# Kernel optimization log

Hardware: AMD Instinct MI355X
Metric: run time of the kernel (lower is better)

The kernel has to match this reference:

```python
import jax, jax.numpy as jnp
import numpy as np

B, T, L, H = 512, 512, 64, 512  # batch, time_steps, sequence_len, hidden_dim


def gru_cell(x, h, W_ih, W_hh, b_ih, b_hh):
    # PyTorch GRUCell math. W_ih: [3H, in], W_hh: [3H, H]; gate order (r, z, n).
    gi = x @ W_ih.T + b_ih
    gh = h @ W_hh.T + b_hh
    i_r, i_z, i_n = jnp.split(gi, 3, axis=-1)
    h_r, h_z, h_n = jnp.split(gh, 3, axis=-1)
    r = jax.nn.sigmoid(i_r + h_r)
    z = jax.nn.sigmoid(i_z + h_z)
    n = jnp.tanh(i_n + r * h_n)
    return (1.0 - z) * n + z * h


def setup_inputs() -> dict:
    key = jax.random.key(0)
    ks = jax.random.split(key, 12)
    s = 1.0 / np.sqrt(H)  # PyTorch GRUCell/Linear init scale
    u = lambda k, shape: jax.random.uniform(k, shape, jnp.float32, -s, s)
    return {
        "x": jax.random.normal(ks[0], (B, T + L - 1), jnp.float32),
        "h_1": jnp.zeros((B, H), jnp.float32),
        "h_2": jnp.zeros((B, H), jnp.float32),
        "W_ih1": u(ks[1], (3 * H, T)),
        "W_hh1": u(ks[2], (3 * H, H)),
        "b_ih1": u(ks[3], (3 * H,)),
        "b_hh1": u(ks[4], (3 * H,)),
        "W_ih2": u(ks[5], (3 * H, H)),
        "W_hh2": u(ks[6], (3 * H, H)),
        "b_ih2": u(ks[7], (3 * H,)),
        "b_hh2": u(ks[8], (3 * H,)),
        "W_fc": u(ks[9], (1, H)),
        "b_fc": u(ks[10], (1,)),
    }


def reference(x, h_1, h_2, W_ih1, W_hh1, b_ih1, b_hh1,
              W_ih2, W_hh2, b_ih2, b_hh2, W_fc, b_fc):
    # Sliding windows x[:, t:t+T] for t in [0, L): gather once, scan over steps.
    idx = jnp.arange(L)[:, None] + jnp.arange(T)[None, :]  # [L, T]
    xs = jnp.transpose(x[:, idx], (1, 0, 2))  # [L, B, T]

    def step(carry, x_t):
        h1, h2 = carry
        h1 = gru_cell(x_t, h1, W_ih1, W_hh1, b_ih1, b_hh1)
        h2 = gru_cell(h1, h2, W_ih2, W_hh2, b_ih2, b_hh2)
        y = (h2 @ W_fc.T + b_fc)[:, 0]  # [B]
        return (h1, h2), y

    (h1, h2), ys = jax.lax.scan(step, (h_1, h_2), xs)
    return ys.T, h1, h2  # output_seq [B, L], final hidden states
```

## Files before the change

kernel.cpp:

```cpp
#include <hip/hip_runtime.h>
#include <hip/hip_bf16.h>
#include <math.h>

typedef __attribute__((ext_vector_type(8))) short short8;
typedef __attribute__((ext_vector_type(4))) float f32x4;
typedef unsigned short u16;
typedef unsigned int u32;

__device__ __forceinline__ u16 f2bf(float f) {
  union { float f; u32 u; } x; x.f = f;
  return (u16)((x.u + 0x7fffu + ((x.u >> 16) & 1u)) >> 16);
}
__device__ __forceinline__ float sigm(float v) { return 1.0f / (1.0f + __expf(-v)); }

#define MFMA __builtin_amdgcn_mfma_f32_16x16x32_bf16
#define HS 262144

#define LDG16_BODY(FL)                                        \
    "global_load_dwordx4 %0, %16, off " FL "\n\t"             \
    "global_load_dwordx4 %1, %16, off offset:64 " FL "\n\t"   \
    "global_load_dwordx4 %2, %16, off offset:128 " FL "\n\t"  \
    "global_load_dwordx4 %3, %16, off offset:192 " FL "\n\t"  \
    "global_load_dwordx4 %4, %16, off offset:256 " FL "\n\t"  \
    "global_load_dwordx4 %5, %16, off offset:320 " FL "\n\t"  \
    "global_load_dwordx4 %6, %16, off offset:384 " FL "\n\t"  \
    "global_load_dwordx4 %7, %16, off offset:448 " FL "\n\t"  \
    "global_load_dwordx4 %8, %16, off offset:512 " FL "\n\t"  \
    "global_load_dwordx4 %9, %16, off offset:576 " FL "\n\t"  \
    "global_load_dwordx4 %10, %16, off offset:640 " FL "\n\t" \
    "global_load_dwordx4 %11, %16, off offset:704 " FL "\n\t" \
    "global_load_dwordx4 %12, %16, off offset:768 " FL "\n\t" \
    "global_load_dwordx4 %13, %16, off offset:832 " FL "\n\t" \
    "global_load_dwordx4 %14, %16, off offset:896 " FL "\n\t" \
    "global_load_dwordx4 %15, %16, off offset:960 " FL "\n\t" \
    "s_waitcnt vmcnt(0)"
#define LDG16_OPS(a, base)                                                     \
    : "=&v"(a[0]), "=&v"(a[1]), "=&v"(a[2]), "=&v"(a[3]), "=&v"(a[4]),         \
      "=&v"(a[5]), "=&v"(a[6]), "=&v"(a[7]), "=&v"(a[8]), "=&v"(a[9]),         \
      "=&v"(a[10]), "=&v"(a[11]), "=&v"(a[12]), "=&v"(a[13]), "=&v"(a[14]),    \
      "=&v"(a[15])                                                             \
    : "v"(base) : "memory"

__device__ __forceinline__ void ldg16_sc0(short8 a[16], const u16* base) {
  asm volatile(LDG16_BODY("sc0") LDG16_OPS(a, base));
}
__device__ __forceinline__ void ldg16_sc01(short8 a[16], const u16* base) {
  asm volatile(LDG16_BODY("sc0 sc1") LDG16_OPS(a, base));
}
__device__ __forceinline__ void stg_sc01(u32* p, u32 v) {
  asm volatile("global_store_dword %0, %1, off sc0 sc1" :: "v"(p), "v"(v) : "memory");
}

__device__ __forceinline__ void waits_nf(unsigned* a, unsigned ta, unsigned* b, unsigned tb) {
  if (threadIdx.x == 0) {
    while (__hip_atomic_load(a, __ATOMIC_RELAXED, __HIP_MEMORY_SCOPE_AGENT) < ta)
      __builtin_amdgcn_s_sleep(1);
    while (__hip_atomic_load(b, __ATOMIC_RELAXED, __HIP_MEMORY_SCOPE_AGENT) < tb)
      __builtin_amdgcn_s_sleep(1);
  }
  __syncthreads();
}

__global__ __launch_bounds__(256, 1) void gru_fused(
    const float* __restrict__ xin, const float* __restrict__ h1in, const float* __restrict__ h2in,
    const float* __restrict__ Wih1, const float* __restrict__ Whh1,
    const float* __restrict__ bih1, const float* __restrict__ bhh1,
    const float* __restrict__ Wih2, const float* __restrict__ Whh2,
    const float* __restrict__ bih2, const float* __restrict__ bhh2,
    const float* __restrict__ Wfc, const float* __restrict__ bfc,
    float* __restrict__ out, u16* __restrict__ wsb, unsigned* __restrict__ barc)
{
  const int bid   = blockIdx.x;
  const int rb    = bid & 3;
  const int layer = (bid >> 2) & 1;
  const int cbl   = bid >> 3;
  const int n0    = cbl * 16;
  const int wid   = bid >> 2;
  const int tid   = threadIdx.x;
  const int w     = tid >> 6;
  const int lane  = tid & 63;
  const int quad  = lane >> 4;
  const int m16   = lane & 15;

  u16* x0  = wsb;
  u16* x1  = x0 + 512 * 576;
  u16* h1r = x1 + 512 * 576;
  u16* h2r = h1r + 4 * HS;
  u16* h1m = h2r + 4 * HS;

  __shared__ short8 wlds[96 * 64];

  unsigned* c0    = barc + rb * 32;
  unsigned* c1    = barc + 256 + rb * 32;
  unsigned* cinit = barc + 512;

  const float* Wih = layer ? Wih2 : Wih1;
  const float* Whh = layer ? Whh2 : Whh1;
  const float* bih = layer ? bih2 : bih1;
  const float* bhh = layer ? bhh2 : bhh1;

  for (int i = wid * 256 + tid; i < 128 * 575; i += 64 * 256) {
    int r = i / 575, c = i - r * 575;
    int row = rb * 128 + r;
    u16 bv = f2bf(xin[row * 575 + c]);
    x0[row * 576 + c] = bv;
    if (c >= 1) x1[row * 576 + (c - 1)] = bv;
  }
  for (int i = wid * 256 + tid; i < 128 * 512; i += 64 * 256) {
    int r = i >> 9, c = i & 511;
    int row = rb * 128 + r;
    u16 h1v = f2bf(h1in[row * 512 + c]);
    h1r[3 * HS + row * 512 + c] = h1v;
    h2r[3 * HS + row * 512 + c] = f2bf(h2in[row * 512 + c]);
  }
  for (int i = tid; i < 96 * 64; i += 256) {
    int blk = i >> 6, l = i & 63;
    int s, gr;
    if (blk < 64) { s = blk & 31; gr = (blk >> 5) * 512; }
    else          { s = blk - 64; gr = 1024; }
    int n  = n0 + (l & 15);
    int k0 = s * 32 + (l >> 4) * 8;
    short8 pk;
    #pragma unroll
    for (int j = 0; j < 8; ++j) {
      int k = k0 + j;
      float v = (k < 512) ? Wih[(gr + n) * 512 + k] : Whh[(gr + n) * 512 + (k - 512)];
      pk[j] = (short)f2bf(v);
    }
    wlds[blk * 64 + l] = pk;
  }

  float hreg[2][4];
  const float* hin = layer ? h2in : h1in;
  #pragma unroll
  for (int rf = 0; rf < 2; ++rf)
    #pragma unroll
    for (int q = 0; q < 4; ++q)
      hreg[rf][q] = hin[(rb * 128 + (2 * w + rf) * 16 + quad * 4 + q) * 512 + n0 + m16];

  const int nn = n0 + m16;
  const float bias_r  = bih[nn] + bhh[nn];
  const float bias_z  = bih[512 + nn] + bhh[512 + nn];
  const float bias_in = bih[1024 + nn];
  const float bias_hn = bhh[1024 + nn];
  const float wfc  = Wfc[nn];
  const float bfcv = bfc[0];

  __syncthreads();
  if (tid == 0) {
    __builtin_amdgcn_fence(__ATOMIC_RELEASE, "agent");
    __hip_atomic_fetch_add(cinit, 1u, __ATOMIC_RELAXED, __HIP_MEMORY_SCOPE_AGENT);
    while (__hip_atomic_load(cinit, __ATOMIC_RELAXED, __HIP_MEMORY_SCOPE_AGENT) < 256u)
      __builtin_amdgcn_s_sleep(1);
    __builtin_amdgcn_fence(__ATOMIC_ACQUIRE, "agent");
  }
  __syncthreads();

  const int arow0 = rb * 128 + (2 * w) * 16 + m16;
  const int arow1 = arow0 + 16;

  if (layer == 0) {
    for (int u = 0; u < 64; ++u) {
      f32x4 acc[2][4] = {};
      {
        const int c = u & 1;
        const u16* xc = c ? x1 : x0;
        const u32* pa0 = (const u32*)(xc + (size_t)arow0 * 576 + (u - c) + quad * 8);
        const u32* pa1 = (const u32*)(xc + (size_t)arow1 * 576 + (u - c) + quad * 8);
        #pragma unroll
        for (int s = 0; s < 16; ++s) {
          union { short8 v; u32 u4[4]; } a0, a1;
          #pragma unroll
          for (int j = 0; j < 4; ++j) { a0.u4[j] = pa0[s * 16 + j]; a1.u4[j] = pa1[s * 16 + j]; }
          short8 br = wlds[(s)      * 64 + lane];
          short8 bz = wlds[(32 + s) * 64 + lane];
          short8 bi = wlds[(64 + s) * 64 + lane];
          acc[0][0] = MFMA(a0.v, br, acc[0][0], 0, 0, 0);
          acc[1][0] = MFMA(a1.v, br, acc[1][0], 0, 0, 0);
          acc[0][1] = MFMA(a0.v, bz, acc[0][1], 0, 0, 0);
          acc[1][1] = MFMA(a1.v, bz, acc[1][1], 0, 0, 0);
          acc[0][2] = MFMA(a0.v, bi, acc[0][2], 0, 0, 0);
          acc[1][2] = MFMA(a1.v, bi, acc[1][2], 0, 0, 0);
        }
      }
      waits_nf(c0, 32u * (unsigned)u, c1, u >= 4 ? 32u * (unsigned)(u - 3) : 0u);
      #pragma unroll
      for (int rf = 0; rf < 2; ++rf) {
        short8 a[16];
        const u16* base = h1r + (size_t)((u + 3) & 3) * HS +
                          (size_t)(rf ? arow1 : arow0) * 512 + quad * 8;
        ldg16_sc0(a, base);
        #pragma unroll
        for (int s = 0; s < 16; ++s) {
          short8 br = wlds[(16 + s) * 64 + lane];
          short8 bz = wlds[(48 + s) * 64 + lane];
          short8 bh = wlds[(80 + s) * 64 + lane];
          acc[rf][0] = MFMA(a[s], br, acc[rf][0], 0, 0, 0);
          acc[rf][1] = MFMA(a[s], bz, acc[rf][1], 0, 0, 0);
          acc[rf][3] = MFMA(a[s], bh, acc[rf][3], 0, 0, 0);
        }
      }
      {
        u16* hw = h1r + (size_t)(u & 3) * HS;
        u32* hm = (u32*)(h1m + (size_t)(u & 3) * HS);
        #pragma unroll
        for (int rf = 0; rf < 2; ++rf)
          #pragma unroll
          for (int q = 0; q < 4; ++q) {
            float rg = sigm(acc[rf][0][q] + bias_r);
            float zg = sigm(acc[rf][1][q] + bias_z);
            float ng = tanhf(acc[rf][2][q] + bias_in + rg * (acc[rf][3][q] + bias_hn));
            float hv = (1.0f - zg) * ng + zg * hreg[rf][q];
            hreg[rf][q] = hv;
            int row = rb * 128 + (2 * w + rf) * 16 + quad * 4 + q;
            u16 b = f2bf(hv);
            hw[row * 512 + nn] = b;
            int pb = __shfl_xor((int)(u32)b, 1);
            if (!(m16 & 1))
              stg_sc01(&hm[(row * 512 + nn) >> 1], (u32)b | ((u32)(u16)pb << 16));
          }
      }
      asm volatile("s_waitcnt vmcnt(0)" ::: "memory");
      __syncthreads();
      if (tid == 0)
        __hip_atomic_fetch_add(c0, 1u, __ATOMIC_RELAXED, __HIP_MEMORY_SCOPE_AGENT);
    }
  } else {
    for (int v = 0; v < 64; ++v) {
      f32x4 acc[2][4] = {};
      waits_nf(c1, 32u * (unsigned)v, c0, 32u * (unsigned)(v + 1));
      #pragma unroll
      for (int rf = 0; rf < 2; ++rf) {
        short8 a[16];
        const u16* base = h2r + (size_t)((v + 3) & 3) * HS +
                          (size_t)(rf ? arow1 : arow0) * 512 + quad * 8;
        ldg16_sc0(a, base);
        #pragma unroll
        for (int s = 0; s < 16; ++s) {
          short8 br = wlds[(16 + s) * 64 + lane];
          short8 bz = wlds[(48 + s) * 64 + lane];
          short8 bh = wlds[(80 + s) * 64 + lane];
          acc[rf][0] = MFMA(a[s], br, acc[rf][0], 0, 0, 0);
          acc[rf][1] = MFMA(a[s], bz, acc[rf][1], 0, 0, 0);
          acc[rf][3] = MFMA(a[s], bh, acc[rf][3], 0, 0, 0);
        }
      }
      #pragma unroll
      for (int rf = 0; rf < 2; ++rf) {
        short8 a[16];
        const u16* base = h1m + (size_t)(v & 3) * HS +
                          (size_t)(rf ? arow1 : arow0) * 512 + quad * 8;
        ldg16_sc01(a, base);
        #pragma unroll
        for (int s = 0; s < 16; ++s) {
          short8 br = wlds[(s)      * 64 + lane];
          short8 bz = wlds[(32 + s) * 64 + lane];
          short8 bi = wlds[(64 + s) * 64 + lane];
          acc[rf][0] = MFMA(a[s], br, acc[rf][0], 0, 0, 0);
          acc[rf][1] = MFMA(a[s], bz, acc[rf][1], 0, 0, 0);
          acc[rf][2] = MFMA(a[s], bi, acc[rf][2], 0, 0, 0);
        }
      }
      {
        u16* hw = h2r + (size_t)(v & 3) * HS;
        #pragma unroll
        for (int rf = 0; rf < 2; ++rf)
          #pragma unroll
          for (int q = 0; q < 4; ++q) {
            float rg = sigm(acc[rf][0][q] + bias_r);
            float zg = sigm(acc[rf][1][q] + bias_z);
            float ng = tanhf(acc[rf][2][q] + bias_in + rg * (acc[rf][3][q] + bias_hn));
            float hv = (1.0f - zg) * ng + zg * hreg[rf][q];
            hreg[rf][q] = hv;
            int row = rb * 128 + (2 * w + rf) * 16 + quad * 4 + q;
            hw[row * 512 + nn] = f2bf(hv);
          }
      }
      __syncthreads();
      if (tid == 0)
        __hip_atomic_fetch_add(c1, 1u, __ATOMIC_RELAXED, __HIP_MEMORY_SCOPE_AGENT);
      #pragma unroll
      for (int rf = 0; rf < 2; ++rf)
        #pragma unroll
        for (int q = 0; q < 4; ++q) {
          float yv = hreg[rf][q] * wfc;
          yv += __shfl_xor(yv, 1);
          yv += __shfl_xor(yv, 2);
          yv += __shfl_xor(yv, 4);
          yv += __shfl_xor(yv, 8);
          if (m16 == 0) {
            int row = rb * 128 + (2 * w + rf) * 16 + quad * 4 + q;
            atomicAdd(&out[row * 64 + v], yv + (n0 == 0 ? bfcv : 0.0f));
          }
        }
    }
  }

  float* hout = out + 32768 + layer * (512 * 512);
  #pragma unroll
  for (int rf = 0; rf < 2; ++rf)
    #pragma unroll
    for (int q = 0; q < 4; ++q) {
      int row = rb * 128 + (2 * w + rf) * 16 + quad * 4 + q;
      hout[row * 512 + nn] = hreg[rf][q];
    }
}

extern "C" void kernel_launch(void* const* d_in, const int* in_sizes, int n_in,
                              void* d_out, int out_size, void* d_ws, size_t ws_size,
                              hipStream_t stream) {
  (void)in_sizes; (void)n_in; (void)out_size; (void)ws_size;
  hipMemsetAsync(d_out, 0, 32768 * sizeof(float), stream);
  hipMemsetAsync(d_ws, 0, 4096, stream);
  unsigned* bar = (unsigned*)d_ws;
  u16* wsb = (u16*)((char*)d_ws + 4096);
  gru_fused<<<256, 256, 0, stream>>>(
      (const float*)d_in[0], (const float*)d_in[1], (const float*)d_in[2],
      (const float*)d_in[3], (const float*)d_in[4], (const float*)d_in[5], (const float*)d_in[6],
      (const float*)d_in[7], (const float*)d_in[8], (const float*)d_in[9], (const float*)d_in[10],
      (const float*)d_in[11], (const float*)d_in[12],
      (float*)d_out, wsb, bar);
}
```

Measured before the change: 806.8 us.

## Pack barrier counters, stage hidden stores via LDS, replace output atomics with partial-sum buffer

Puts the two per-row-block step counters side by side so one 64-bit load checks both, and every thread polls it instead of thread 0 plus a block barrier. Each step's new hidden state is staged through shared memory so it can be written with 16-byte stores instead of scattered 2-byte and 4-byte stores. The per-step output atomicAdds are replaced by per-column-block partial dot products written to a workspace buffer, which a final grid barrier reduces into the output; this also drops the output memset. The cost is extra LDS traffic, a wait on outstanding stores in layer 2, and a closing grid-wide barrier plus a reduction pass.

```diff
diff --git a/kernel.cpp b/kernel.cpp
--- a/kernel.cpp
+++ b/kernel.cpp
@@ -4,12 +4,17 @@
 
 typedef __attribute__((ext_vector_type(8))) short short8;
 typedef __attribute__((ext_vector_type(4))) float f32x4;
+typedef __attribute__((ext_vector_type(4))) int i32x4;
 typedef unsigned short u16;
 typedef unsigned int u32;
+typedef unsigned long long u64;
 
 __device__ __forceinline__ u16 f2bf(float f) {
   union { float f; u32 u; } x; x.f = f;
   return (u16)((x.u + 0x7fffu + ((x.u >> 16) & 1u)) >> 16);
+}
+__device__ __forceinline__ float bf2f(u32 bits) {
+  union { u32 u; float f; } x; x.u = bits; return x.f;
 }
 __device__ __forceinline__ float sigm(float v) { return 1.0f / (1.0f + __expf(-v)); }
 
@@ -47,18 +52,19 @@
 __device__ __forceinline__ void ldg16_sc01(short8 a[16], const u16* base) {
   asm volatile(LDG16_BODY("sc0 sc1") LDG16_OPS(a, base));
 }
-__device__ __forceinline__ void stg_sc01(u32* p, u32 v) {
+__device__ __forceinline__ void stg4_sc01(void* p, i32x4 v) {
+  asm volatile("global_store_dwordx4 %0, %1, off sc0 sc1" :: "v"(p), "v"(v) : "memory");
+}
+__device__ __forceinline__ void stg1_sc01(void* p, u32 v) {
   asm volatile("global_store_dword %0, %1, off sc0 sc1" :: "v"(p), "v"(v) : "memory");
 }
 
-__device__ __forceinline__ void waits_nf(unsigned* a, unsigned ta, unsigned* b, unsigned tb) {
-  if (threadIdx.x == 0) {
-    while (__hip_atomic_load(a, __ATOMIC_RELAXED, __HIP_MEMORY_SCOPE_AGENT) < ta)
-      __builtin_amdgcn_s_sleep(1);
-    while (__hip_atomic_load(b, __ATOMIC_RELAXED, __HIP_MEMORY_SCOPE_AGENT) < tb)
-      __builtin_amdgcn_s_sleep(1);
-  }
-  __syncthreads();
+__device__ __forceinline__ void waitpair(const u64* p, u32 tlo, u32 thi) {
+  while (true) {
+    u64 v = __hip_atomic_load(p, __ATOMIC_RELAXED, __HIP_MEMORY_SCOPE_AGENT);
+    if ((u32)v >= tlo && (u32)(v >> 32) >= thi) return;
+    __builtin_amdgcn_s_sleep(1);
+  }
 }
 
 __global__ __launch_bounds__(256, 1) void gru_fused(
@@ -87,12 +93,16 @@
   u16* h1r = x1 + 512 * 576;
   u16* h2r = h1r + 4 * HS;
   u16* h1m = h2r + 4 * HS;
+  u32* ysl = (u32*)(h1m + 4 * HS);
 
   __shared__ short8 wlds[96 * 64];
-
-  unsigned* c0    = barc + rb * 32;
-  unsigned* c1    = barc + 256 + rb * 32;
-  unsigned* cinit = barc + 512;
+  __shared__ u32 stage[4 * 288];
+
+  u64* pair = (u64*)(barc + rb * 16);
+  u32* c0   = (u32*)pair;
+  u32* c1   = c0 + 1;
+  u32* cinit = barc + 128;
+  u32* cfin  = barc + 132;
 
   const float* Wih = layer ? Wih2 : Wih1;
   const float* Whh = layer ? Whh2 : Whh1;
@@ -109,8 +119,7 @@
   for (int i = wid * 256 + tid; i < 128 * 512; i += 64 * 256) {
     int r = i >> 9, c = i & 511;
     int row = rb * 128 + r;
-    u16 h1v = f2bf(h1in[row * 512 + c]);
-    h1r[3 * HS + row * 512 + c] = h1v;
+    h1r[3 * HS + row * 512 + c] = f2bf(h1in[row * 512 + c]);
     h2r[3 * HS + row * 512 + c] = f2bf(h2in[row * 512 + c]);
   }
   for (int i = tid; i < 96 * 64; i += 256) {
@@ -143,8 +152,10 @@
   const float bias_z  = bih[512 + nn] + bhh[512 + nn];
   const float bias_in = bih[1024 + nn];
   const float bias_hn = bhh[1024 + nn];
-  const float wfc  = Wfc[nn];
   const float bfcv = bfc[0];
+  float wfc8[8];
+  #pragma unroll
+  for (int k = 0; k < 8; ++k) wfc8[k] = Wfc[n0 + (lane & 1) * 8 + k];
 
   __syncthreads();
   if (tid == 0) {
@@ -158,6 +169,9 @@
 
   const int arow0 = rb * 128 + (2 * w) * 16 + m16;
   const int arow1 = arow0 + 16;
+  const int rl    = lane >> 1;
+  const int hl    = lane & 1;
+  const int growt = rb * 128 + w * 32 + rl;
 
   if (layer == 0) {
     for (int u = 0; u < 64; ++u) {
@@ -183,7 +197,7 @@
           acc[1][2] = MFMA(a1.v, bi, acc[1][2], 0, 0, 0);
         }
       }
-      waits_nf(c0, 32u * (unsigned)u, c1, u >= 4 ? 32u * (unsigned)(u - 3) : 0u);
+      waitpair(pair, 32u * (unsigned)u, u >= 4 ? 32u * (unsigned)(u - 3) : 0u);
       #pragma unroll
       for (int rf = 0; rf < 2; ++rf) {
         short8 a[16];
@@ -200,25 +214,29 @@
           acc[rf][3] = MFMA(a[s], bh, acc[rf][3], 0, 0, 0);
         }
       }
+      #pragma unroll
+      for (int rf = 0; rf < 2; ++rf)
+        #pragma unroll
+        for (int q = 0; q < 4; ++q) {
+          float rg = sigm(acc[rf][0][q] + bias_r);
+          float zg = sigm(acc[rf][1][q] + bias_z);
+          float ng = tanhf(acc[rf][2][q] + bias_in + rg * (acc[rf][3][q] + bias_hn));
+          float hv = (1.0f - zg) * ng + zg * hreg[rf][q];
+          hreg[rf][q] = hv;
+          u16 b = f2bf(hv);
+          u32 pv = (u32)b | ((u32)(u16)__shfl_xor((int)b, 1) << 16);
+          if (!(m16 & 1))
+            stage[w * 288 + (rf * 16 + quad * 4 + q) * 9 + (m16 >> 1)] = pv;
+        }
       {
-        u16* hw = h1r + (size_t)(u & 3) * HS;
-        u32* hm = (u32*)(h1m + (size_t)(u & 3) * HS);
-        #pragma unroll
-        for (int rf = 0; rf < 2; ++rf)
-          #pragma unroll
-          for (int q = 0; q < 4; ++q) {
-            float rg = sigm(acc[rf][0][q] + bias_r);
-            float zg = sigm(acc[rf][1][q] + bias_z);
-            float ng = tanhf(acc[rf][2][q] + bias_in + rg * (acc[rf][3][q] + bias_hn));
-            float hv = (1.0f - zg) * ng + zg * hreg[rf][q];
-            hreg[rf][q] = hv;
-            int row = rb * 128 + (2 * w + rf) * 16 + quad * 4 + q;
-            u16 b = f2bf(hv);
-            hw[row * 512 + nn] = b;
-            int pb = __shfl_xor((int)(u32)b, 1);
-            if (!(m16 & 1))
-              stg_sc01(&hm[(row * 512 + nn) >> 1], (u32)b | ((u32)(u16)pb << 16));
-          }
+        i32x4 dv;
+        dv.x = (int)stage[w * 288 + rl * 9 + hl * 4 + 0];
+        dv.y = (int)stage[w * 288 + rl * 9 + hl * 4 + 1];
+        dv.z = (int)stage[w * 288 + rl * 9 + hl * 4 + 2];
+        dv.w = (int)stage[w * 288 + rl * 9 + hl * 4 + 3];
+        size_t off = (size_t)(u & 3) * HS + (size_t)growt * 512 + n0 + hl * 8;
+        *(i32x4*)(h1r + off) = dv;
+        stg4_sc01(h1m + off, dv);
       }
       asm volatile("s_waitcnt vmcnt(0)" ::: "memory");
       __syncthreads();
@@ -228,7 +246,7 @@
   } else {
     for (int v = 0; v < 64; ++v) {
       f32x4 acc[2][4] = {};
-      waits_nf(c1, 32u * (unsigned)v, c0, 32u * (unsigned)(v + 1));
+      waitpair(pair, 32u * (unsigned)(v + 1), 32u * (unsigned)v);
       #pragma unroll
       for (int rf = 0; rf < 2; ++rf) {
         short8 a[16];
@@ -261,38 +279,45 @@
           acc[rf][2] = MFMA(a[s], bi, acc[rf][2], 0, 0, 0);
         }
       }
+      #pragma unroll
+      for (int rf = 0; rf < 2; ++rf)
+        #pragma unroll
+        for (int q = 0; q < 4; ++q) {
+          float rg = sigm(acc[rf][0][q] + bias_r);
+          float zg = sigm(acc[rf][1][q] + bias_z);
+          float ng = tanhf(acc[rf][2][q] + bias_in + rg * (acc[rf][3][q] + bias_hn));
+          float hv = (1.0f - zg) * ng + zg * hreg[rf][q];
+          hreg[rf][q] = hv;
+          u16 b = f2bf(hv);
+          u32 pv = (u32)b | ((u32)(u16)__shfl_xor((int)b, 1) << 16);
+          if (!(m16 & 1))
+            stage[w * 288 + (rf * 16 + quad * 4 + q) * 9 + (m16 >> 1)] = pv;
+        }
       {
-        u16* hw = h2r + (size_t)(v & 3) * HS;
-        #pragma unroll
-        for (int rf = 0; rf < 2; ++rf)
-          #pragma unroll
-          for (int q = 0; q < 4; ++q) {
-            float rg = sigm(acc[rf][0][q] + bias_r);
-            float zg = sigm(acc[rf][1][q] + bias_z);
-            float ng = tanhf(acc[rf][2][q] + bias_in + rg * (acc[rf][3][q] + bias_hn));
-            float hv = (1.0f - zg) * ng + zg * hreg[rf][q];
-            hreg[rf][q] = hv;
-            int row = rb * 128 + (2 * w + rf) * 16 + quad * 4 + q;
-            hw[row * 512 + nn] = f2bf(hv);
-          }
-      }
+        i32x4 dv;
+        dv.x = (int)stage[w * 288 + rl * 9 + hl * 4 + 0];
+        dv.y = (int)stage[w * 288 + rl * 9 + hl * 4 + 1];
+        dv.z = (int)stage[w * 288 + rl * 9 + hl * 4 + 2];
+        dv.w = (int)stage[w * 288 + rl * 9 + hl * 4 + 3];
+        size_t off = (size_t)(v & 3) * HS + (size_t)growt * 512 + n0 + hl * 8;
+        *(i32x4*)(h2r + off) = dv;
+        float yl = 0.0f;
+        u32 dd[4] = {(u32)dv.x, (u32)dv.y, (u32)dv.z, (u32)dv.w};
+        #pragma unroll
+        for (int j = 0; j < 4; ++j) {
+          yl += bf2f(dd[j] << 16) * wfc8[2 * j];
+          yl += bf2f(dd[j] & 0xffff0000u) * wfc8[2 * j + 1];
+        }
+        yl += __shfl_xor(yl, 1);
+        if (!hl) {
+          union { float f; u32 u; } yu; yu.f = yl;
+          stg1_sc01(ysl + ((size_t)(cbl * 512 + growt) * 64 + v), yu.u);
+        }
+      }
+      asm volatile("s_waitcnt vmcnt(0)" ::: "memory");
       __syncthreads();
       if (tid == 0)
         __hip_atomic_fetch_add(c1, 1u, __ATOMIC_RELAXED, __HIP_MEMORY_SCOPE_AGENT);
-      #pragma unroll
-      for (int rf = 0; rf < 2; ++rf)
-        #pragma unroll
-        for (int q = 0; q < 4; ++q) {
-          float yv = hreg[rf][q] * wfc;
-          yv += __shfl_xor(yv, 1);
-          yv += __shfl_xor(yv, 2);
-          yv += __shfl_xor(yv, 4);
-          yv += __shfl_xor(yv, 8);
-          if (m16 == 0) {
-            int row = rb * 128 + (2 * w + rf) * 16 + quad * 4 + q;
-            atomicAdd(&out[row * 64 + v], yv + (n0 == 0 ? bfcv : 0.0f));
-          }
-        }
     }
   }
 
@@ -304,14 +329,34 @@
       int row = rb * 128 + (2 * w + rf) * 16 + quad * 4 + q;
       hout[row * 512 + nn] = hreg[rf][q];
     }
+
+  asm volatile("s_waitcnt vmcnt(0)" ::: "memory");
+  __syncthreads();
+  if (tid == 0)
+    __hip_atomic_fetch_add(cfin, 1u, __ATOMIC_RELAXED, __HIP_MEMORY_SCOPE_AGENT);
+  while (__hip_atomic_load(cfin, __ATOMIC_RELAXED, __HIP_MEMORY_SCOPE_AGENT) < 256u)
+    __builtin_amdgcn_s_sleep(1);
+
+  if (tid < 128) {
+    int row = 2 * bid + (tid >> 6);
+    int t   = tid & 63;
+    float acc = bfcv;
+    #pragma unroll
+    for (int cb = 0; cb < 32; ++cb) {
+      u32 bits = __hip_atomic_load(ysl + ((size_t)(cb * 512 + row) * 64 + t),
+                                   __ATOMIC_RELAXED, __HIP_MEMORY_SCOPE_AGENT);
+      union { u32 u; float f; } cv; cv.u = bits;
+      acc += cv.f;
+    }
+    out[row * 64 + t] = acc;
+  }
 }
 
 extern "C" void kernel_launch(void* const* d_in, const int* in_sizes, int n_in,
                               void* d_out, int out_size, void* d_ws, size_t ws_size,
                               hipStream_t stream) {
   (void)in_sizes; (void)n_in; (void)out_size; (void)ws_size;
-  hipMemsetAsync(d_out, 0, 32768 * sizeof(float), stream);
-  hipMemsetAsync(d_ws, 0, 4096, stream);
+  (void)hipMemsetAsync(d_ws, 0, 4096, stream);
   unsigned* bar = (unsigned*)d_ws;
   u16* wsb = (u16*)((char*)d_ws + 4096);
   gru_fused<<<256, 256, 0, stream>>>(
```

New measurement: 930.9 us. 15.4% more time.
